# Performance work log

Hardware: AMD Instinct MI355X
Metric: run time of the kernel (lower is better)

Reference implementation:

```python
import jax, jax.numpy as jnp
import numpy as np

EPS_BN = 1e-5
SLOPE = 0.2
K_SCALES = (5, 20, 30)
K_BRANCH = 20


def _pairwise(x):
    # x: [B, C, N] -> negative squared distances [B, N, N]
    inner = -2.0 * jnp.einsum('bcn,bcm->bnm', x, x)
    xx = jnp.sum(x * x, axis=1)  # [B, N]
    return -xx[:, :, None] - inner - xx[:, None, :]


def _gather(xt, idx):
    # xt: [B, N, C], idx: [B, N, k] -> [B, N, k, C]
    B = xt.shape[0]
    return xt[jnp.arange(B)[:, None, None], idx]


def _bn(x, g, b):
    # eval-mode BN: running_mean=0, running_var=1
    sh = (1, -1) + (1,) * (x.ndim - 2)
    return x * (g / jnp.sqrt(1.0 + EPS_BN)).reshape(sh) + b.reshape(sh)


def _conv(x, w, g, b):
    # 1x1 conv (no bias) + BN + LeakyReLU; x: [B, Cin, ...], w: [Cout, Cin]
    y = jnp.einsum('oc,bc...->bo...', w, x)
    return jax.nn.leaky_relu(_bn(y, g, b), SLOPE)


def _edge_feature(x, k):
    # DGCNN edge feature: cat(neighbor - center, center) -> [B, 2C, N, k]
    idx = jax.lax.top_k(_pairwise(x), k)[1]
    xt = jnp.transpose(x, (0, 2, 1))  # [B, N, C]
    nb = _gather(xt, idx)             # [B, N, k, C]
    ctr = jnp.broadcast_to(xt[:, :, None, :], nb.shape)
    return jnp.transpose(jnp.concatenate([nb - ctr, ctr], axis=-1), (0, 3, 1, 2))


def _hierarchical_features(x):
    pd = _pairwise(x)
    xt = jnp.transpose(x, (0, 2, 1))  # [B, N, 3]
    feats = []
    for scale, k in enumerate(K_SCALES):
        idx = jax.lax.top_k(pd, k)[1]
        nb = _gather(xt, idx)
        ctr = jnp.broadcast_to(xt[:, :, None, :], nb.shape)
        rel = nb - ctr
        if scale == 0:
            f = jnp.concatenate([rel, ctr], axis=-1)                         # 6 ch
        elif scale == 1:
            n = jnp.linalg.norm(rel, axis=-1, keepdims=True) + 1e-8
            f = jnp.concatenate([rel, rel / n, ctr], axis=-1)                # 9 ch
        else:
            d = jnp.linalg.norm(rel, axis=-1, keepdims=True)
            f = jnp.concatenate([rel, ctr, d], axis=-1)                      # 7 ch
        feats.append(jnp.transpose(f, (0, 3, 1, 2)))  # [B, C, N, k]
    return feats


def _forward(x, w1l, g1l, b1l, w1b, g1b, b1b, w1c, g1c, b1c,
             wf, gf, bf, w2, g2, b2, w3, g3, b3, w4, g4, b4,
             w5, g5, b5, wl1, g6, b6, wl2, bl2, g7, b7, wl3, bl3):
    fL, fB, fC = _hierarchical_features(x)
    xl = jnp.max(_conv(fL, w1l, g1l, b1l), axis=-1)   # [B, 64, N]
    xb = jnp.max(_conv(fB, w1b, g1b, b1b), axis=-1)
    xc = jnp.max(_conv(fC, w1c, g1c, b1c), axis=-1)
    xm = jnp.concatenate([xl, xb, xc], axis=1)        # [B, 192, N]
    x1 = _conv(xm, wf, gf, bf)                        # [B, 64, N]
    e = _edge_feature(x1, K_BRANCH)
    x2 = jnp.max(_conv(e, w2, g2, b2), axis=-1)       # [B, 64, N]
    e = _edge_feature(x2, K_BRANCH)
    x3 = jnp.max(_conv(e, w3, g3, b3), axis=-1)       # [B, 128, N]
    e = _edge_feature(x3, K_BRANCH)
    x4 = jnp.max(_conv(e, w4, g4, b4), axis=-1)       # [B, 256, N]
    xcat = jnp.concatenate([x1, x2, x3, x4], axis=1)  # [B, 512, N]
    x5 = _conv(xcat, w5, g5, b5)                      # [B, emb, N]
    h = jnp.concatenate([jnp.max(x5, axis=-1), jnp.mean(x5, axis=-1)], axis=1)  # [B, 2*emb]
    h = jax.nn.leaky_relu(_bn(h @ wl1.T, g6, b6), SLOPE)          # [B, 512]
    h = jax.nn.leaky_relu(_bn(h @ wl2.T + bl2, g7, b7), SLOPE)    # [B, 256]
    return h @ wl3.T + bl3                                        # [B, 7]


def setup_inputs() -> dict:
    key = jax.random.key(0)
    ks = jax.random.split(key, 64)
    it = iter(range(64))
    def W(shape):
        return 0.05 * jax.random.normal(ks[next(it)], shape, jnp.float32)
    def G(n):
        return 1.0 + 0.1 * jax.random.normal(ks[next(it)], (n,), jnp.float32)
    def Bt(n):
        return 0.1 * jax.random.normal(ks[next(it)], (n,), jnp.float32)
    emb = 1024
    inp = {
        'x': jax.random.normal(ks[next(it)], (16, 3, 2048), jnp.float32),
        'w1l': W((64, 6)),  'g1l': G(64),  'b1l': Bt(64),
        'w1b': W((64, 9)),  'g1b': G(64),  'b1b': Bt(64),
        'w1c': W((64, 7)),  'g1c': G(64),  'b1c': Bt(64),
        'wf': W((64, 192)), 'gf': G(64),   'bf': Bt(64),
        'w2': W((64, 128)), 'g2': G(64),   'b2': Bt(64),
        'w3': W((128, 128)),'g3': G(128),  'b3': Bt(128),
        'w4': W((256, 256)),'g4': G(256),  'b4': Bt(256),
        'w5': W((emb, 512)),'g5': G(emb),  'b5': Bt(emb),
        'wl1': W((512, 2 * emb)), 'g6': G(512), 'b6': Bt(512),
        'wl2': W((256, 512)), 'bl2': Bt(256), 'g7': G(256), 'b7': Bt(256),
        'wl3': W((7, 256)), 'bl3': Bt(7),
    }
    return inp


def reference(x, w1l, g1l, b1l, w1b, g1b, b1b, w1c, g1c, b1c,
              wf, gf, bf, w2, g2, b2, w3, g3, b3, w4, g4, b4,
              w5, g5, b5, wl1, g6, b6, wl2, bl2, g7, b7, wl3, bl3):
    return _forward(x, w1l, g1l, b1l, w1b, g1b, b1b, w1c, g1c, b1c,
                    wf, gf, bf, w2, g2, b2, w3, g3, b3, w4, g4, b4,
                    w5, g5, b5, wl1, g6, b6, wl2, bl2, g7, b7, wl3, bl3)
```

## Files before the change

### kernel.cpp

```cpp
#include <hip/hip_runtime.h>
#include <math.h>

#define BB 16
#define NN 2048
#define BN (BB * NN)
#define XS 512

typedef unsigned short u16;
typedef __attribute__((ext_vector_type(8))) short short8;
typedef __attribute__((ext_vector_type(4))) float f32x4;

__device__ __forceinline__ float leaky(float z) { return z > 0.f ? z : 0.2f * z; }
__device__ __forceinline__ float bnscale(float g) { return g / sqrtf(1.f + 1e-5f); }

template<int K>
__device__ __forceinline__ void wave_topk(float lv[32], int lane, int* out) {
    unsigned pop = 0u;
    float b1 = -INFINITY, b2 = -INFINITY;
    int j1 = 0, j2 = 0;
    #pragma unroll
    for (int m = 0; m < 32; ++m) {
        float v = lv[m];
        bool c1 = v > b1, c2 = v > b2;
        b2 = c1 ? b1 : (c2 ? v : b2);
        j2 = c1 ? j1 : (c2 ? m : j2);
        b1 = c1 ? v : b1;
        j1 = c1 ? m : j1;
    }
    bool stale = false;
    #pragma unroll 1
    for (int k = 0; k < K; ++k) {
        float wv = b1; int wj = j1 * 64 + lane;
        #pragma unroll
        for (int off = 1; off < 64; off <<= 1) {
            float ov = __shfl_xor(wv, off);
            int   oj = __shfl_xor(wj, off);
            if (ov > wv || (ov == wv && oj < wj)) { wv = ov; wj = oj; }
        }
        if (lane == 0) out[k] = wj;
        if (j1 * 64 + lane == wj) {
            pop |= 1u << j1;
            if (stale) {
                b1 = -INFINITY; b2 = -INFINITY; j1 = 0; j2 = 0;
                #pragma unroll
                for (int m = 0; m < 32; ++m) {
                    float v = ((pop >> m) & 1u) ? -INFINITY : lv[m];
                    bool c1 = v > b1, c2 = v > b2;
                    b2 = c1 ? b1 : (c2 ? v : b2);
                    j2 = c1 ? j1 : (c2 ? m : j2);
                    b1 = c1 ? v : b1;
                    j1 = c1 ? m : j1;
                }
                stale = false;
            } else {
                b1 = b2; j1 = j2;
                stale = true;
            }
        }
    }
}

__global__ __launch_bounds__(256) void topk_xyz(const float* __restrict__ x,
                                                int* __restrict__ idx30) {
    const int tile = blockIdx.x;
    const int b = tile >> 9;
    const int i0 = (tile & 511) * 4;
    __shared__ float dist[4][NN];
    const float* xb = x + (size_t)b * 3 * NN;
    float xi[4][3], ni[4];
    #pragma unroll
    for (int t = 0; t < 4; ++t) {
        xi[t][0] = xb[i0 + t];
        xi[t][1] = xb[NN + i0 + t];
        xi[t][2] = xb[2 * NN + i0 + t];
        ni[t] = xi[t][0] * xi[t][0] + xi[t][1] * xi[t][1] + xi[t][2] * xi[t][2];
    }
    for (int j = threadIdx.x; j < NN; j += 256) {
        float a0 = xb[j], a1 = xb[NN + j], a2 = xb[2 * NN + j];
        float nj = a0 * a0 + a1 * a1 + a2 * a2;
        #pragma unroll
        for (int t = 0; t < 4; ++t) {
            float dot = xi[t][0] * a0 + xi[t][1] * a1 + xi[t][2] * a2;
            dist[t][j] = 2.f * dot - ni[t] - nj;
        }
    }
    __syncthreads();
    const int w = threadIdx.x >> 6;
    const int lane = threadIdx.x & 63;
    float lv[32];
    #pragma unroll
    for (int m = 0; m < 32; ++m) lv[m] = dist[w][m * 64 + lane];
    wave_topk<30>(lv, lane, idx30 + ((size_t)b * NN + i0 + w) * 30);
}

__global__ __launch_bounds__(64) void hier_conv(
        const float* __restrict__ x, const int* __restrict__ idx30,
        const float* __restrict__ w1l, const float* __restrict__ g1l, const float* __restrict__ b1l,
        const float* __restrict__ w1b, const float* __restrict__ g1b, const float* __restrict__ b1b,
        const float* __restrict__ w1c, const float* __restrict__ g1c, const float* __restrict__ b1c,
        const float* __restrict__ wf,  const float* __restrict__ gf,  const float* __restrict__ bf_,
        float* __restrict__ x1out) {
    const int bi = blockIdx.x;
    const int b = bi >> 11;
    const int i = bi & (NN - 1);
    const int o = threadIdx.x;
    __shared__ float xm[192];
    __shared__ float xjs[30][3];
    const float* xb = x + (size_t)b * 3 * NN;
    float xi0 = xb[i], xi1 = xb[NN + i], xi2 = xb[2 * NN + i];
    if (o < 30) {
        int j = idx30[(size_t)bi * 30 + o];
        xjs[o][0] = xb[j]; xjs[o][1] = xb[NN + j]; xjs[o][2] = xb[2 * NN + j];
    }
    float wl[6], wb[9], wc[7];
    #pragma unroll
    for (int c = 0; c < 6; ++c) wl[c] = w1l[o * 6 + c];
    #pragma unroll
    for (int c = 0; c < 9; ++c) wb[c] = w1b[o * 9 + c];
    #pragma unroll
    for (int c = 0; c < 7; ++c) wc[c] = w1c[o * 7 + c];
    float sl = bnscale(g1l[o]), bl = b1l[o];
    float sb = bnscale(g1b[o]), bbv = b1b[o];
    float sc = bnscale(g1c[o]), bc = b1c[o];
    __syncthreads();
    float aL = -INFINITY, aB = -INFINITY, aC = -INFINITY;
    for (int k = 0; k < 30; ++k) {
        float r0 = xjs[k][0] - xi0, r1 = xjs[k][1] - xi1, r2 = xjs[k][2] - xi2;
        float ss = r0 * r0 + r1 * r1 + r2 * r2;
        if (k < 5) {
            float y = wl[0]*r0 + wl[1]*r1 + wl[2]*r2 + wl[3]*xi0 + wl[4]*xi1 + wl[5]*xi2;
            aL = fmaxf(aL, leaky(y * sl + bl));
        }
        if (k < 20) {
            float nrm = sqrtf(ss) + 1e-8f;
            float y = wb[0]*r0 + wb[1]*r1 + wb[2]*r2
                    + wb[3]*(r0/nrm) + wb[4]*(r1/nrm) + wb[5]*(r2/nrm)
                    + wb[6]*xi0 + wb[7]*xi1 + wb[8]*xi2;
            aB = fmaxf(aB, leaky(y * sb + bbv));
        }
        {
            float d = sqrtf(ss);
            float y = wc[0]*r0 + wc[1]*r1 + wc[2]*r2 + wc[3]*xi0 + wc[4]*xi1 + wc[5]*xi2 + wc[6]*d;
            aC = fmaxf(aC, leaky(y * sc + bc));
        }
    }
    xm[o] = aL; xm[64 + o] = aB; xm[128 + o] = aC;
    __syncthreads();
    const float* wr = wf + (size_t)o * 192;
    float y = 0.f;
    #pragma unroll 8
    for (int c = 0; c < 192; c += 4) {
        float4 wv = *(const float4*)(wr + c);
        float4 xv = *(const float4*)(&xm[c]);
        y += wv.x * xv.x + wv.y * xv.y + wv.z * xv.z + wv.w * xv.w;
    }
    y = leaky(y * bnscale(gf[o]) + bf_[o]);
    x1out[(size_t)bi * XS + o] = y;
}

template<int C>
__global__ __launch_bounds__(256) void rownorm(const float* __restrict__ xin,
                                               float* __restrict__ nrm) {
    int i = blockIdx.x * 256 + threadIdx.x;
    const float* r = xin + (size_t)i * XS;
    float s = 0.f;
    #pragma unroll 4
    for (int c = 0; c < C; c += 4) {
        float4 v = *(const float4*)(r + c);
        s += v.x * v.x + v.y * v.y + v.z * v.z + v.w * v.w;
    }
    nrm[i] = s;
}

template<int C>
__global__ __launch_bounds__(256) void transpose_feat(const float* __restrict__ xin,
                                                      float* __restrict__ xT) {
    const int blk = blockIdx.x;
    const int b = blk >> 5;
    const int i0 = (blk & 31) * 64;
    const int it = threadIdx.x & 63;
    const int cg = threadIdx.x >> 6;
    const int i = i0 + it;
    const float* row = xin + (size_t)(b * NN + i) * XS;
    float* xTb = xT + (size_t)b * C * NN;
    #pragma unroll 1
    for (int c = cg * (C / 4); c < (cg + 1) * (C / 4); c += 4) {
        float4 v = *(const float4*)(row + c);
        xTb[(size_t)(c + 0) * NN + i] = v.x;
        xTb[(size_t)(c + 1) * NN + i] = v.y;
        xTb[(size_t)(c + 2) * NN + i] = v.z;
        xTb[(size_t)(c + 3) * NN + i] = v.w;
    }
}

template<int C>
__global__ __launch_bounds__(256, 2) void topk_feat(const float* __restrict__ xin,
                                                    const float* __restrict__ nrm,
                                                    int* __restrict__ idx20) {
    const int i0 = blockIdx.x * 8;
    const int b = i0 >> 11;
    const int li0 = i0 & (NN - 1);
    __shared__ float dist[8][NN];
    const int tid = threadIdx.x;
    const float* xb = xin + (size_t)b * NN * XS;
    const float* xi_g = xb + (size_t)li0 * XS;
    float ni[8];
    #pragma unroll
    for (int t = 0; t < 8; ++t) ni[t] = nrm[b * NN + li0 + t];
    #pragma unroll 1
    for (int s = 0; s < 2; ++s) {
        const int j0 = tid + 1024 * s;
        float nj[4];
        #pragma unroll
        for (int q = 0; q < 4; ++q) nj[q] = nrm[b * NN + j0 + 256 * q];
        float acc[8][4];
        #pragma unroll
        for (int t = 0; t < 8; ++t)
            #pragma unroll
            for (int q = 0; q < 4; ++q) acc[t][q] = 0.f;
        #pragma unroll 1
        for (int c = 0; c < C; c += 16) {
            float4 v[4][4];
            #pragma unroll
            for (int q = 0; q < 4; ++q) {
                const float* xj = xb + (size_t)(j0 + 256 * q) * XS + c;
                v[q][0] = *(const float4*)(xj);
                v[q][1] = *(const float4*)(xj + 4);
                v[q][2] = *(const float4*)(xj + 8);
                v[q][3] = *(const float4*)(xj + 12);
            }
            #pragma unroll
            for (int t = 0; t < 8; ++t) {
                const float* xr = xi_g + (size_t)t * XS + c;
                float4 a0 = *(const float4*)(xr);
                float4 a1 = *(const float4*)(xr + 4);
                float4 a2 = *(const float4*)(xr + 8);
                float4 a3 = *(const float4*)(xr + 12);
                #pragma unroll
                for (int q = 0; q < 4; ++q) {
                    float sum = acc[t][q];
                    sum += a0.x * v[q][0].x; sum += a0.y * v[q][0].y;
                    sum += a0.z * v[q][0].z; sum += a0.w * v[q][0].w;
                    sum += a1.x * v[q][1].x; sum += a1.y * v[q][1].y;
                    sum += a1.z * v[q][1].z; sum += a1.w * v[q][1].w;
                    sum += a2.x * v[q][2].x; sum += a2.y * v[q][2].y;
                    sum += a2.z * v[q][2].z; sum += a2.w * v[q][2].w;
                    sum += a3.x * v[q][3].x; sum += a3.y * v[q][3].y;
                    sum += a3.z * v[q][3].z; sum += a3.w * v[q][3].w;
                    acc[t][q] = sum;
                }
            }
        }
        #pragma unroll
        for (int t = 0; t < 8; ++t)
            #pragma unroll
            for (int q = 0; q < 4; ++q)
                dist[t][j0 + 256 * q] = 2.f * acc[t][q] - ni[t] - nj[q];
    }
    __syncthreads();
    const int w = tid >> 6;
    const int lane = tid & 63;
    #pragma unroll 1
    for (int rr = 0; rr < 2; ++rr) {
        const int t = w + 4 * rr;
        float lv[32];
        #pragma unroll
        for (int m = 0; m < 32; ++m) lv[m] = dist[t][m * 64 + lane];
        wave_topk<20>(lv, lane, idx20 + (size_t)(i0 + t) * 20);
    }
}

template<int C>
__global__ __launch_bounds__(256, 4) void topk_feat_t(
        const float* __restrict__ xin, const float* __restrict__ xT,
        const float* __restrict__ nrm, int* __restrict__ idx20) {
    const int i0 = blockIdx.x * 8;
    const int b = i0 >> 11;
    const int li0 = i0 & (NN - 1);
    __shared__ float dist[4][NN];
    __shared__ float xi[8][C];
    const int tid = threadIdx.x;
    for (int t4 = tid * 4; t4 < 8 * C; t4 += 1024) {
        const int t = t4 / C, c = t4 % C;
        *(float4*)&xi[t][c] = *(const float4*)&xin[(size_t)(i0 + t) * XS + c];
    }
    float4 nj[2];
    #pragma unroll
    for (int q = 0; q < 2; ++q)
        nj[q] = *(const float4*)&nrm[b * NN + q * 1024 + tid * 4];
    const float* xTb = xT + (size_t)b * C * NN;
    __syncthreads();
    const int w = tid >> 6;
    const int lane = tid & 63;
    #pragma unroll 1
    for (int hh = 0; hh < 2; ++hh) {
        const int ib = hh * 4;
        float ni[4];
        #pragma unroll
        for (int t = 0; t < 4; ++t) ni[t] = nrm[b * NN + li0 + ib + t];
        float acc[4][8];
        #pragma unroll
        for (int t = 0; t < 4; ++t)
            #pragma unroll
            for (int j = 0; j < 8; ++j) acc[t][j] = 0.f;
        #pragma unroll 1
        for (int c0 = 0; c0 < C; c0 += 4) {
            float4 vj[2][4];
            #pragma unroll
            for (int q = 0; q < 2; ++q)
                #pragma unroll
                for (int cc = 0; cc < 4; ++cc)
                    vj[q][cc] = *(const float4*)&xTb[(size_t)(c0 + cc) * NN
                                                     + q * 1024 + tid * 4];
            #pragma unroll
            for (int t = 0; t < 4; ++t) {
                const float4 av = *(const float4*)&xi[ib + t][c0];
                #pragma unroll
                for (int q = 0; q < 2; ++q) {
                    acc[t][q*4+0] += av.x * vj[q][0].x;
                    acc[t][q*4+1] += av.x * vj[q][0].y;
                    acc[t][q*4+2] += av.x * vj[q][0].z;
                    acc[t][q*4+3] += av.x * vj[q][0].w;
                    acc[t][q*4+0] += av.y * vj[q][1].x;
                    acc[t][q*4+1] += av.y * vj[q][1].y;
                    acc[t][q*4+2] += av.y * vj[q][1].z;
                    acc[t][q*4+3] += av.y * vj[q][1].w;
                    acc[t][q*4+0] += av.z * vj[q][2].x;
                    acc[t][q*4+1] += av.z * vj[q][2].y;
                    acc[t][q*4+2] += av.z * vj[q][2].z;
                    acc[t][q*4+3] += av.z * vj[q][2].w;
                    acc[t][q*4+0] += av.w * vj[q][3].x;
                    acc[t][q*4+1] += av.w * vj[q][3].y;
                    acc[t][q*4+2] += av.w * vj[q][3].z;
                    acc[t][q*4+3] += av.w * vj[q][3].w;
                }
            }
        }
        if (hh) __syncthreads();
        #pragma unroll
        for (int tt = 0; tt < 4; ++tt) {
            #pragma unroll
            for (int q = 0; q < 2; ++q) {
                float4 d;
                d.x = 2.f * acc[tt][q*4+0] - ni[tt] - nj[q].x;
                d.y = 2.f * acc[tt][q*4+1] - ni[tt] - nj[q].y;
                d.z = 2.f * acc[tt][q*4+2] - ni[tt] - nj[q].z;
                d.w = 2.f * acc[tt][q*4+3] - ni[tt] - nj[q].w;
                *(float4*)&dist[tt][q * 1024 + tid * 4] = d;
            }
        }
        __syncthreads();
        float lv[32];
        #pragma unroll
        for (int m = 0; m < 32; ++m) lv[m] = dist[w][m * 64 + lane];
        wave_topk<20>(lv, lane, idx20 + (size_t)(i0 + ib + w) * 20);
    }
}

template<int C, int COUT>
__global__ __launch_bounds__(256) void pconv(
        const float* __restrict__ xin,
        const float* __restrict__ w,
        float* __restrict__ pt) {
    constexpr int O2 = 2 * COUT;
    constexpr int PB = 8192 / O2;
    constexpr int OG = O2 / 8;
    constexpr int PG = PB / 4;
    static_assert(OG * PG == 256, "tile mismatch");
    const int i0 = blockIdx.x * PB;
    __shared__ __align__(16) float xt[PB][C + 4];
    const int tid = threadIdx.x;
    for (int t = tid * 4; t < PB * C; t += 1024)
        *(float4*)(&xt[t / C][t % C]) =
            *(const float4*)(&xin[(size_t)(i0 + t / C) * XS + (t % C)]);
    __syncthreads();
    const int og = tid % OG, pg = tid / OG;
    const int o0 = og * 8, p0 = pg * 4;
    const bool thalf = (o0 >= COUT);
    const float* wb0 = w + (size_t)(thalf ? o0 - COUT : o0) * 2 * C;
    float acc[8][4];
    #pragma unroll
    for (int r = 0; r < 8; ++r)
        #pragma unroll
        for (int p = 0; p < 4; ++p) acc[r][p] = 0.f;
    #pragma unroll 2
    for (int c = 0; c < C; c += 4) {
        float4 wf[8];
        if (thalf) {
            #pragma unroll
            for (int r = 0; r < 8; ++r) {
                float4 a = *(const float4*)(wb0 + (size_t)r * 2 * C + c);
                float4 bq = *(const float4*)(wb0 + (size_t)r * 2 * C + C + c);
                wf[r].x = bq.x - a.x; wf[r].y = bq.y - a.y;
                wf[r].z = bq.z - a.z; wf[r].w = bq.w - a.w;
            }
        } else {
            #pragma unroll
            for (int r = 0; r < 8; ++r)
                wf[r] = *(const float4*)(wb0 + (size_t)r * 2 * C + c);
        }
        #pragma unroll
        for (int p = 0; p < 4; ++p) {
            float4 xv = *(const float4*)(&xt[p0 + p][c]);
            #pragma unroll
            for (int r = 0; r < 8; ++r)
                acc[r][p] += wf[r].x * xv.x + wf[r].y * xv.y
                           + wf[r].z * xv.z + wf[r].w * xv.w;
        }
    }
    #pragma unroll
    for (int p = 0; p < 4; ++p) {
        float* dst = pt + (size_t)(i0 + p0 + p) * O2 + o0;
        *(float4*)(dst)     = make_float4(acc[0][p], acc[1][p], acc[2][p], acc[3][p]);
        *(float4*)(dst + 4) = make_float4(acc[4][p], acc[5][p], acc[6][p], acc[7][p]);
    }
}

template<int COUT>
__global__ __launch_bounds__(256) void gmax(
        const float* __restrict__ pt, const int* __restrict__ idx20,
        const float* __restrict__ g, const float* __restrict__ bb,
        float* __restrict__ xout) {
    constexpr int TPP = COUT / 4;
    constexpr int PTS = 256 / TPP;
    const int i0 = blockIdx.x * PTS;
    const int base = i0 & ~(NN - 1);
    __shared__ int jl[PTS][20];
    const int tid = threadIdx.x;
    for (int t = tid; t < PTS * 20; t += 256)
        jl[t / 20][t % 20] = idx20[(size_t)(i0 + t / 20) * 20 + (t % 20)];
    __syncthreads();
    const int p = tid / TPP;
    const int q = (tid % TPP) * 4;
    const int i = i0 + p;
    float4 mx = make_float4(-INFINITY, -INFINITY, -INFINITY, -INFINITY);
    float4 mn = make_float4(INFINITY, INFINITY, INFINITY, INFINITY);
    #pragma unroll 4
    for (int k = 0; k < 20; ++k) {
        float4 v = *(const float4*)(pt + (size_t)(base + jl[p][k]) * (2 * COUT) + q);
        mx.x = fmaxf(mx.x, v.x); mx.y = fmaxf(mx.y, v.y);
        mx.z = fmaxf(mx.z, v.z); mx.w = fmaxf(mx.w, v.w);
        mn.x = fminf(mn.x, v.x); mn.y = fminf(mn.y, v.y);
        mn.z = fminf(mn.z, v.z); mn.w = fminf(mn.w, v.w);
    }
    float4 tv = *(const float4*)(pt + (size_t)i * (2 * COUT) + COUT + q);
    float4 gv = *(const float4*)(g + q);
    float4 bv = *(const float4*)(bb + q);
    float4 res;
    {
        float s = bnscale(gv.x); res.x = leaky(((s >= 0.f ? mx.x : mn.x) + tv.x) * s + bv.x);
    }{
        float s = bnscale(gv.y); res.y = leaky(((s >= 0.f ? mx.y : mn.y) + tv.y) * s + bv.y);
    }{
        float s = bnscale(gv.z); res.z = leaky(((s >= 0.f ? mx.z : mn.z) + tv.z) * s + bv.z);
    }{
        float s = bnscale(gv.w); res.w = leaky(((s >= 0.f ? mx.w : mn.w) + tv.w) * s + bv.w);
    }
    *(float4*)(xout + (size_t)i * XS + q) = res;
}

__global__ __launch_bounds__(256) void split_bf16(const float* __restrict__ in,
                                                  u16* __restrict__ hi,
                                                  u16* __restrict__ lo, int n4) {
    int i = blockIdx.x * 256 + threadIdx.x;
    if (i >= n4) return;
    float4 v = ((const float4*)in)[i];
    float vv[4] = {v.x, v.y, v.z, v.w};
    unsigned h[4], l[4];
    #pragma unroll
    for (int t = 0; t < 4; ++t) {
        unsigned u = __float_as_uint(vv[t]);
        unsigned r = (u + 0x7FFFu + ((u >> 16) & 1u)) >> 16;
        h[t] = r;
        float res = vv[t] - __uint_as_float(r << 16);
        unsigned u2 = __float_as_uint(res);
        l[t] = (u2 + 0x7FFFu + ((u2 >> 16) & 1u)) >> 16;
    }
    ((uint2*)hi)[i] = make_uint2(h[0] | (h[1] << 16), h[2] | (h[3] << 16));
    ((uint2*)lo)[i] = make_uint2(l[0] | (l[1] << 16), l[2] | (l[3] << 16));
}

__global__ __launch_bounds__(256) void conv5_mfma2(
        const u16* __restrict__ xhi, const u16* __restrict__ xlo,
        const u16* __restrict__ whi, const u16* __restrict__ wlo,
        const float* __restrict__ g5, const float* __restrict__ b5,
        float* __restrict__ pmax, float* __restrict__ psum) {
    const int mblk = blockIdx.x >> 2;
    const int nblk = blockIdx.x & 3;
    const int wv = threadIdx.x >> 6;
    const int lane = threadIdx.x & 63;
    const int row = lane & 15;
    const int quad = lane >> 4;
    const int m0 = mblk * 64;
    const int n0 = nblk * 256 + wv * 64;
    const u16* xh = xhi + (size_t)(m0 + row) * 512 + quad * 8;
    const u16* xl = xlo + (size_t)(m0 + row) * 512 + quad * 8;
    const u16* wh = whi + (size_t)(n0 + row) * 512 + quad * 8;
    const u16* wl = wlo + (size_t)(n0 + row) * 512 + quad * 8;
    f32x4 acc[4][4];
    #pragma unroll
    for (int f = 0; f < 4; ++f)
        #pragma unroll
        for (int g = 0; g < 4; ++g) acc[f][g] = (f32x4){0.f, 0.f, 0.f, 0.f};
    #pragma unroll 1
    for (int k = 0; k < 512; k += 32) {
        short8 ah[4], al[4], bh[4], bl[4];
        #pragma unroll
        for (int f = 0; f < 4; ++f) {
            ah[f] = *(const short8*)(xh + (size_t)f * 16 * 512 + k);
            al[f] = *(const short8*)(xl + (size_t)f * 16 * 512 + k);
        }
        #pragma unroll
        for (int g = 0; g < 4; ++g) {
            bh[g] = *(const short8*)(wh + (size_t)g * 16 * 512 + k);
            bl[g] = *(const short8*)(wl + (size_t)g * 16 * 512 + k);
        }
        #pragma unroll
        for (int f = 0; f < 4; ++f)
            #pragma unroll
            for (int g = 0; g < 4; ++g) {
                acc[f][g] = __builtin_amdgcn_mfma_f32_16x16x32_bf16(ah[f], bh[g], acc[f][g], 0, 0, 0);
                acc[f][g] = __builtin_amdgcn_mfma_f32_16x16x32_bf16(ah[f], bl[g], acc[f][g], 0, 0, 0);
                acc[f][g] = __builtin_amdgcn_mfma_f32_16x16x32_bf16(al[f], bh[g], acc[f][g], 0, 0, 0);
            }
    }
    const int b = m0 >> 11;
    const int ch0 = (m0 & (NN - 1)) >> 4;
    #pragma unroll
    for (int f = 0; f < 4; ++f) {
        const int ch = ch0 + f;
        #pragma unroll
        for (int g = 0; g < 4; ++g) {
            const int oc = n0 + g * 16 + row;
            float s = bnscale(g5[oc]), bv = b5[oc];
            float mx = -INFINITY, sm = 0.f;
            #pragma unroll
            for (int r = 0; r < 4; ++r) {
                float z = leaky(acc[f][g][r] * s + bv);
                mx = fmaxf(mx, z); sm += z;
            }
            mx = fmaxf(mx, __shfl_xor(mx, 16)); sm += __shfl_xor(sm, 16);
            mx = fmaxf(mx, __shfl_xor(mx, 32)); sm += __shfl_xor(sm, 32);
            if (lane < 16) {
                pmax[((size_t)b * 128 + ch) * 1024 + oc] = mx;
                psum[((size_t)b * 128 + ch) * 1024 + oc] = sm;
            }
        }
    }
}

__global__ __launch_bounds__(256, 3) void conv5_pool(
        const float* __restrict__ xcat,
        const float* __restrict__ w5, const float* __restrict__ g5,
        const float* __restrict__ b5,
        float* __restrict__ pmax, float* __restrict__ psum) {
    const int blk = blockIdx.x;
    const int b = blk >> 6;
    const int ch = blk & 63;
    const int i0 = ch * 32;
    const float* xrow = xcat + ((size_t)b * NN + i0) * XS;
    const int tid = threadIdx.x;
    float acc[4][32];
    #pragma unroll
    for (int q = 0; q < 4; ++q)
        #pragma unroll
        for (int p = 0; p < 32; ++p) acc[q][p] = 0.f;
    #pragma unroll 1
    for (int c = 0; c < 512; c += 4) {
        float4 wv[4];
        #pragma unroll
        for (int q = 0; q < 4; ++q)
            wv[q] = *(const float4*)(w5 + (size_t)(tid + 256 * q) * 512 + c);
        #pragma unroll
        for (int p = 0; p < 32; ++p) {
            float4 xs = *(const float4*)(xrow + (size_t)p * XS + c);
            #pragma unroll
            for (int q = 0; q < 4; ++q)
                acc[q][p] += wv[q].x * xs.x + wv[q].y * xs.y
                           + wv[q].z * xs.z + wv[q].w * xs.w;
        }
    }
    #pragma unroll
    for (int q = 0; q < 4; ++q) {
        int oc = tid + 256 * q;
        float s = bnscale(g5[oc]), bv = b5[oc];
        float m = -INFINITY, sm = 0.f;
        #pragma unroll
        for (int p = 0; p < 32; ++p) {
            float z = leaky(acc[q][p] * s + bv);
            m = fmaxf(m, z);
            sm += z;
        }
        pmax[((size_t)b * 64 + ch) * 1024 + oc] = m;
        psum[((size_t)b * 64 + ch) * 1024 + oc] = sm;
    }
}

__global__ __launch_bounds__(256) void pool_reduce(
        const float* __restrict__ pmax, const float* __restrict__ psum,
        int nch, float* __restrict__ hbuf) {
    const int b = blockIdx.x >> 3;
    const int g = blockIdx.x & 7;
    const int tid = threadIdx.x;
    const int oc = g * 128 + (tid & 127);
    const int half = tid >> 7;
    const int h0 = half * (nch / 2);
    float m = -INFINITY, sm = 0.f;
    for (int ch = h0; ch < h0 + nch / 2; ++ch) {
        m = fmaxf(m, pmax[((size_t)b * nch + ch) * 1024 + oc]);
        sm += psum[((size_t)b * nch + ch) * 1024 + oc];
    }
    __shared__ float sx[128], ss[128];
    if (half == 1) { sx[tid & 127] = m; ss[tid & 127] = sm; }
    __syncthreads();
    if (half == 0) {
        m = fmaxf(m, sx[tid & 127]);
        sm += ss[tid & 127];
        hbuf[(size_t)b * 2048 + oc] = m;
        hbuf[(size_t)b * 2048 + 1024 + oc] = sm * (1.0f / 2048.0f);
    }
}

__global__ __launch_bounds__(256) void fc_head(
        const float* __restrict__ hbuf,
        const float* __restrict__ wl1, const float* __restrict__ g6, const float* __restrict__ b6,
        const float* __restrict__ wl2, const float* __restrict__ bl2,
        const float* __restrict__ g7, const float* __restrict__ b7,
        const float* __restrict__ wl3, const float* __restrict__ bl3,
        float* __restrict__ out) {
    const int b = blockIdx.x;
    const int tid = threadIdx.x;
    __shared__ float h[2048];
    __shared__ float h1[512];
    __shared__ float h2[256];
    for (int t = tid * 4; t < 2048; t += 1024)
        *(float4*)(&h[t]) = *(const float4*)(hbuf + (size_t)b * 2048 + t);
    __syncthreads();
    #pragma unroll
    for (int q = 0; q < 2; ++q) {
        int o = tid + 256 * q;
        const float* wr = wl1 + (size_t)o * 2048;
        float y = 0.f;
        for (int c = 0; c < 2048; c += 4) {
            float4 wv = *(const float4*)(wr + c);
            float4 hv = *(const float4*)(&h[c]);
            y += wv.x * hv.x + wv.y * hv.y + wv.z * hv.z + wv.w * hv.w;
        }
        y = y * bnscale(g6[o]) + b6[o];
        h1[o] = leaky(y);
    }
    __syncthreads();
    {
        int o = tid;
        const float* wr = wl2 + (size_t)o * 512;
        float y = 0.f;
        for (int c = 0; c < 512; c += 4) {
            float4 wv = *(const float4*)(wr + c);
            float4 hv = *(const float4*)(&h1[c]);
            y += wv.x * hv.x + wv.y * hv.y + wv.z * hv.z + wv.w * hv.w;
        }
        y = (y + bl2[o]) * bnscale(g7[o]) + b7[o];
        h2[o] = leaky(y);
    }
    __syncthreads();
    if (tid < 7) {
        const float* wr = wl3 + tid * 256;
        float y = 0.f;
        for (int c = 0; c < 256; ++c) y += wr[c] * h2[c];
        out[b * 7 + tid] = y + bl3[tid];
    }
}

extern "C" void kernel_launch(void* const* d_in, const int* in_sizes, int n_in,
                              void* d_out, int out_size, void* d_ws, size_t ws_size,
                              hipStream_t stream) {
    const float* x   = (const float*)d_in[0];
    const float* w1l = (const float*)d_in[1];
    const float* g1l = (const float*)d_in[2];
    const float* b1l = (const float*)d_in[3];
    const float* w1b = (const float*)d_in[4];
    const float* g1b = (const float*)d_in[5];
    const float* b1b = (const float*)d_in[6];
    const float* w1c = (const float*)d_in[7];
    const float* g1c = (const float*)d_in[8];
    const float* b1c = (const float*)d_in[9];
    const float* wf  = (const float*)d_in[10];
    const float* gf  = (const float*)d_in[11];
    const float* bf_ = (const float*)d_in[12];
    const float* w2  = (const float*)d_in[13];
    const float* g2  = (const float*)d_in[14];
    const float* b2  = (const float*)d_in[15];
    const float* w3  = (const float*)d_in[16];
    const float* g3  = (const float*)d_in[17];
    const float* b3  = (const float*)d_in[18];
    const float* w4  = (const float*)d_in[19];
    const float* g4  = (const float*)d_in[20];
    const float* b4  = (const float*)d_in[21];
    const float* w5  = (const float*)d_in[22];
    const float* g5  = (const float*)d_in[23];
    const float* b5  = (const float*)d_in[24];
    const float* wl1 = (const float*)d_in[25];
    const float* g6  = (const float*)d_in[26];
    const float* b6  = (const float*)d_in[27];
    const float* wl2 = (const float*)d_in[28];
    const float* bl2 = (const float*)d_in[29];
    const float* g7  = (const float*)d_in[30];
    const float* b7  = (const float*)d_in[31];
    const float* wl3 = (const float*)d_in[32];
    const float* bl3 = (const float*)d_in[33];
    float* out = (float*)d_out;

    char* ws = (char*)d_ws;
    int*   idxb = (int*)(ws);
    float* xcat = (float*)(ws + ((size_t)4  << 20));
    float* nrm  = (float*)(ws + ((size_t)68 << 20));
    float* hbuf = (float*)(ws + ((size_t)68 << 20) + ((size_t)256 << 10));
    float* pt   = (float*)(ws + ((size_t)69 << 20));
    float* xT   = (float*)(ws + ((size_t)69 << 20));
    const bool mfma_ok = ws_size >= ((size_t)151 << 20);
    u16* xlo = (u16*)(ws + ((size_t)69  << 20));
    u16* xhi = (u16*)(ws + ((size_t)101 << 20));
    u16* whi = (u16*)(ws + ((size_t)133 << 20));
    u16* wlo = (u16*)(ws + ((size_t)134 << 20));
    float* pmax = mfma_ok ? (float*)(ws + ((size_t)135 << 20))
                          : (float*)(ws + ((size_t)69 << 20));
    float* psum = mfma_ok ? (float*)(ws + ((size_t)143 << 20))
                          : (float*)(ws + ((size_t)73 << 20));
    const int nch = mfma_ok ? 128 : 64;
    float* x1 = xcat;
    float* x2 = xcat + 64;
    float* x3 = xcat + 128;
    float* x4 = xcat + 256;

    topk_xyz<<<BB * NN / 4, 256, 0, stream>>>(x, idxb);
    hier_conv<<<BB * NN, 64, 0, stream>>>(x, idxb, w1l, g1l, b1l, w1b, g1b, b1b,
                                          w1c, g1c, b1c, wf, gf, bf_, x1);
    rownorm<64><<<BN / 256, 256, 0, stream>>>(x1, nrm);
    if (mfma_ok) {
        transpose_feat<64><<<BB * 32, 256, 0, stream>>>(x1, xT);
        topk_feat_t<64><<<BN / 8, 256, 0, stream>>>(x1, xT, nrm, idxb);
    } else {
        topk_feat<64><<<BN / 8, 256, 0, stream>>>(x1, nrm, idxb);
    }
    pconv<64, 64><<<BN / 64, 256, 0, stream>>>(x1, w2, pt);
    gmax<64><<<BN / 16, 256, 0, stream>>>(pt, idxb, g2, b2, x2);
    rownorm<64><<<BN / 256, 256, 0, stream>>>(x2, nrm);
    if (mfma_ok) {
        transpose_feat<64><<<BB * 32, 256, 0, stream>>>(x2, xT);
        topk_feat_t<64><<<BN / 8, 256, 0, stream>>>(x2, xT, nrm, idxb);
    } else {
        topk_feat<64><<<BN / 8, 256, 0, stream>>>(x2, nrm, idxb);
    }
    pconv<64, 128><<<BN / 32, 256, 0, stream>>>(x2, w3, pt);
    gmax<128><<<BN / 8, 256, 0, stream>>>(pt, idxb, g3, b3, x3);
    rownorm<128><<<BN / 256, 256, 0, stream>>>(x3, nrm);
    if (mfma_ok) {
        transpose_feat<128><<<BB * 32, 256, 0, stream>>>(x3, xT);
        topk_feat_t<128><<<BN / 8, 256, 0, stream>>>(x3, xT, nrm, idxb);
    } else {
        topk_feat<128><<<BN / 8, 256, 0, stream>>>(x3, nrm, idxb);
    }
    for (int h = 0; h < 2; ++h) {
        pconv<128, 128><<<BN / 32, 256, 0, stream>>>(x3, w4 + (size_t)h * 128 * 256, pt);
        gmax<128><<<BN / 8, 256, 0, stream>>>(pt, idxb, g4 + h * 128, b4 + h * 128,
                                              x4 + h * 128);
    }
    if (mfma_ok) {
        split_bf16<<<(BN * 512 / 4) / 256, 256, 0, stream>>>(xcat, xhi, xlo, BN * 512 / 4);
        split_bf16<<<(1024 * 512 / 4) / 256, 256, 0, stream>>>(w5, whi, wlo, 1024 * 512 / 4);
        conv5_mfma2<<<(BN / 64) * 4, 256, 0, stream>>>(xhi, xlo, whi, wlo,
                                                       g5, b5, pmax, psum);
    } else {
        conv5_pool<<<BB * 64, 256, 0, stream>>>(xcat, w5, g5, b5, pmax, psum);
    }
    pool_reduce<<<BB * 8, 256, 0, stream>>>(pmax, psum, nch, hbuf);
    fc_head<<<BB, 256, 0, stream>>>(hbuf, wl1, g6, b6, wl2, bl2,
                                    g7, b7, wl3, bl3, out);
}
```

Measured before the change: 2.575 ms.

## Process all eight query rows in one pass with 512-thread top-k blocks

The feature-space kNN kernel now uses 512 threads per block, computing distances for all eight query rows in a single pass over the transposed features instead of two passes of four rows. This halves the number of times each block streams the neighbor feature columns from memory, and lets all eight waves run their top-k selection concurrently. Shared memory for the distance buffer doubles, which can lower the number of resident blocks per CU.

```diff
diff --git a/kernel.cpp b/kernel.cpp
--- a/kernel.cpp
+++ b/kernel.cpp
@@ -271,90 +271,73 @@
 }
 
 template<int C>
-__global__ __launch_bounds__(256, 4) void topk_feat_t(
+__global__ __launch_bounds__(512, 4) void topk_feat_t(
         const float* __restrict__ xin, const float* __restrict__ xT,
         const float* __restrict__ nrm, int* __restrict__ idx20) {
     const int i0 = blockIdx.x * 8;
     const int b = i0 >> 11;
     const int li0 = i0 & (NN - 1);
-    __shared__ float dist[4][NN];
+    __shared__ float dist[8][NN];
     __shared__ float xi[8][C];
     const int tid = threadIdx.x;
-    for (int t4 = tid * 4; t4 < 8 * C; t4 += 1024) {
+    for (int t4 = tid * 4; t4 < 8 * C; t4 += 2048) {
         const int t = t4 / C, c = t4 % C;
         *(float4*)&xi[t][c] = *(const float4*)&xin[(size_t)(i0 + t) * XS + c];
     }
-    float4 nj[2];
-    #pragma unroll
-    for (int q = 0; q < 2; ++q)
-        nj[q] = *(const float4*)&nrm[b * NN + q * 1024 + tid * 4];
+    float ni[8];
+    #pragma unroll
+    for (int t = 0; t < 8; ++t) ni[t] = nrm[b * NN + li0 + t];
+    const float4 nj = *(const float4*)&nrm[b * NN + tid * 4];
     const float* xTb = xT + (size_t)b * C * NN;
+    __syncthreads();
+    float acc[8][4];
+    #pragma unroll
+    for (int t = 0; t < 8; ++t)
+        #pragma unroll
+        for (int j = 0; j < 4; ++j) acc[t][j] = 0.f;
+    #pragma unroll 1
+    for (int c0 = 0; c0 < C; c0 += 4) {
+        float4 vj[4];
+        #pragma unroll
+        for (int cc = 0; cc < 4; ++cc)
+            vj[cc] = *(const float4*)&xTb[(size_t)(c0 + cc) * NN + tid * 4];
+        #pragma unroll
+        for (int t = 0; t < 8; ++t) {
+            const float4 av = *(const float4*)&xi[t][c0];
+            acc[t][0] += av.x * vj[0].x;
+            acc[t][1] += av.x * vj[0].y;
+            acc[t][2] += av.x * vj[0].z;
+            acc[t][3] += av.x * vj[0].w;
+            acc[t][0] += av.y * vj[1].x;
+            acc[t][1] += av.y * vj[1].y;
+            acc[t][2] += av.y * vj[1].z;
+            acc[t][3] += av.y * vj[1].w;
+            acc[t][0] += av.z * vj[2].x;
+            acc[t][1] += av.z * vj[2].y;
+            acc[t][2] += av.z * vj[2].z;
+            acc[t][3] += av.z * vj[2].w;
+            acc[t][0] += av.w * vj[3].x;
+            acc[t][1] += av.w * vj[3].y;
+            acc[t][2] += av.w * vj[3].z;
+            acc[t][3] += av.w * vj[3].w;
+        }
+    }
+    #pragma unroll
+    for (int t = 0; t < 8; ++t) {
+        float4 d;
+        d.x = 2.f * acc[t][0] - ni[t] - nj.x;
+        d.y = 2.f * acc[t][1] - ni[t] - nj.y;
+        d.z = 2.f * acc[t][2] - ni[t] - nj.z;
+        d.w = 2.f * acc[t][3] - ni[t] - nj.w;
+        *(float4*)&dist[t][tid * 4] = d;
+    }
     __syncthreads();
     const int w = tid >> 6;
     const int lane = tid & 63;
-    #pragma unroll 1
-    for (int hh = 0; hh < 2; ++hh) {
-        const int ib = hh * 4;
-        float ni[4];
-        #pragma unroll
-        for (int t = 0; t < 4; ++t) ni[t] = nrm[b * NN + li0 + ib + t];
-        float acc[4][8];
-        #pragma unroll
-        for (int t = 0; t < 4; ++t)
-            #pragma unroll
-            for (int j = 0; j < 8; ++j) acc[t][j] = 0.f;
-        #pragma unroll 1
-        for (int c0 = 0; c0 < C; c0 += 4) {
-            float4 vj[2][4];
-            #pragma unroll
-            for (int q = 0; q < 2; ++q)
-                #pragma unroll
-                for (int cc = 0; cc < 4; ++cc)
-                    vj[q][cc] = *(const float4*)&xTb[(size_t)(c0 + cc) * NN
-                                                     + q * 1024 + tid * 4];
-            #pragma unroll
-            for (int t = 0; t < 4; ++t) {
-                const float4 av = *(const float4*)&xi[ib + t][c0];
-                #pragma unroll
-                for (int q = 0; q < 2; ++q) {
-                    acc[t][q*4+0] += av.x * vj[q][0].x;
-                    acc[t][q*4+1] += av.x * vj[q][0].y;
-                    acc[t][q*4+2] += av.x * vj[q][0].z;
-                    acc[t][q*4+3] += av.x * vj[q][0].w;
-                    acc[t][q*4+0] += av.y * vj[q][1].x;
-                    acc[t][q*4+1] += av.y * vj[q][1].y;
-                    acc[t][q*4+2] += av.y * vj[q][1].z;
-                    acc[t][q*4+3] += av.y * vj[q][1].w;
-                    acc[t][q*4+0] += av.z * vj[q][2].x;
-                    acc[t][q*4+1] += av.z * vj[q][2].y;
-                    acc[t][q*4+2] += av.z * vj[q][2].z;
-                    acc[t][q*4+3] += av.z * vj[q][2].w;
-                    acc[t][q*4+0] += av.w * vj[q][3].x;
-                    acc[t][q*4+1] += av.w * vj[q][3].y;
-                    acc[t][q*4+2] += av.w * vj[q][3].z;
-                    acc[t][q*4+3] += av.w * vj[q][3].w;
-                }
-            }
-        }
-        if (hh) __syncthreads();
-        #pragma unroll
-        for (int tt = 0; tt < 4; ++tt) {
-            #pragma unroll
-            for (int q = 0; q < 2; ++q) {
-                float4 d;
-                d.x = 2.f * acc[tt][q*4+0] - ni[tt] - nj[q].x;
-                d.y = 2.f * acc[tt][q*4+1] - ni[tt] - nj[q].y;
-                d.z = 2.f * acc[tt][q*4+2] - ni[tt] - nj[q].z;
-                d.w = 2.f * acc[tt][q*4+3] - ni[tt] - nj[q].w;
-                *(float4*)&dist[tt][q * 1024 + tid * 4] = d;
-            }
-        }
-        __syncthreads();
-        float lv[32];
-        #pragma unroll
-        for (int m = 0; m < 32; ++m) lv[m] = dist[w][m * 64 + lane];
-        wave_topk<20>(lv, lane, idx20 + (size_t)(i0 + ib + w) * 20);
-    }
+    float lv[32];
+    #pragma unroll
+    for (int m = 0; m < 32; ++m) lv[m] = dist[w][m * 64 + lane];
+    wave_topk<20>(lv, lane, idx20 + (size_t)(i0 + w) * 20);
 }
 
 template<int C, int COUT>
@@ -738,7 +721,7 @@
     rownorm<64><<<BN / 256, 256, 0, stream>>>(x1, nrm);
     if (mfma_ok) {
         transpose_feat<64><<<BB * 32, 256, 0, stream>>>(x1, xT);
-        topk_feat_t<64><<<BN / 8, 256, 0, stream>>>(x1, xT, nrm, idxb);
+        topk_feat_t<64><<<BN / 8, 512, 0, stream>>>(x1, xT, nrm, idxb);
     } else {
         topk_feat<64><<<BN / 8, 256, 0, stream>>>(x1, nrm, idxb);
     }
@@ -747,7 +730,7 @@
     rownorm<64><<<BN / 256, 256, 0, stream>>>(x2, nrm);
     if (mfma_ok) {
         transpose_feat<64><<<BB * 32, 256, 0, stream>>>(x2, xT);
-        topk_feat_t<64><<<BN / 8, 256, 0, stream>>>(x2, xT, nrm, idxb);
+        topk_feat_t<64><<<BN / 8, 512, 0, stream>>>(x2, xT, nrm, idxb);
     } else {
         topk_feat<64><<<BN / 8, 256, 0, stream>>>(x2, nrm, idxb);
     }
@@ -756,7 +739,7 @@
     rownorm<128><<<BN / 256, 256, 0, stream>>>(x3, nrm);
     if (mfma_ok) {
         transpose_feat<128><<<BB * 32, 256, 0, stream>>>(x3, xT);
-        topk_feat_t<128><<<BN / 8, 256, 0, stream>>>(x3, xT, nrm, idxb);
+        topk_feat_t<128><<<BN / 8, 512, 0, stream>>>(x3, xT, nrm, idxb);
     } else {
         topk_feat<128><<<BN / 8, 256, 0, stream>>>(x3, nrm, idxb);
     }
```

Measured after the change: 2.545 ms. No clear change (-1.1%).
